# Kernel optimization log

Hardware: AMD Instinct MI355X
Metric: run time of the kernel (lower is better)

The kernel has to match this reference:

```python
import jax, jax.numpy as jnp
import numpy as np

D_IN = 1024
D_OUT = 1024
NUM_HEADS = 16
HEAD_DIM = D_OUT // NUM_HEADS
EPS = 1e-6
POW = 16.0


def setup_inputs() -> dict:
    key = jax.random.key(0)
    ks = jax.random.split(key, 6)
    s = 1.0 / np.sqrt(D_IN)
    x = jax.random.normal(ks[0], (2, 2048, D_IN), dtype=jnp.float32)
    Wq = jax.random.uniform(ks[1], (D_OUT, D_IN), jnp.float32, -s, s)
    Wk = jax.random.uniform(ks[2], (D_OUT, D_IN), jnp.float32, -s, s)
    Wv = jax.random.uniform(ks[3], (D_OUT, D_IN), jnp.float32, -s, s)
    Wo = jax.random.uniform(ks[4], (D_OUT, D_OUT), jnp.float32, -s, s)
    bo = jax.random.uniform(ks[5], (D_OUT,), jnp.float32, -s, s)
    return {"x": x, "Wq": Wq, "Wk": Wk, "Wv": Wv, "Wo": Wo, "bo": bo}


def _l2norm(t):
    # torch F.normalize: t / max(||t||, eps)
    n = jnp.sqrt(jnp.sum(t * t, axis=-1, keepdims=True))
    return t / jnp.maximum(n, EPS)


def reference(x, Wq, Wk, Wv, Wo, bo):
    B, T, _ = x.shape
    # project and split heads: [B, H, T, Dh]
    def heads(W):
        y = jnp.einsum('btd,od->bto', x, W)
        return y.reshape(B, T, NUM_HEADS, HEAD_DIM).transpose(0, 2, 1, 3)
    Q = _l2norm(heads(Wq))
    K = _l2norm(heads(Wk))
    V = heads(Wv)
    cos_sim = jnp.clip(jnp.einsum('bhtd,bhsd->bhts', Q, K), -0.999, 0.999)
    scores = 1.0 - jnp.arccos(cos_sim) / jnp.pi
    W = jnp.power(jnp.maximum(scores, EPS), POW)
    W = W / (jnp.sum(W, axis=-1, keepdims=True) + EPS)
    out = jnp.einsum('bhts,bhsd->bhtd', W, V)
    out = out.transpose(0, 2, 1, 3).reshape(B, T, D_OUT)
    return jnp.einsum('bto,po->btp', out, Wo) + bo
```

## Files before the change

kernel.cpp:

```cpp
#include <hip/hip_runtime.h>
#include <math.h>

constexpr int Dm   = 1024;
constexpr int NH   = 16;
constexpr int HD   = 64;
constexpr int Bb   = 2;
constexpr int Tt   = 2048;
constexpr int MTOT = Bb * Tt;
#define EPSF 1e-6f

typedef __attribute__((ext_vector_type(8))) short short8;
typedef __attribute__((ext_vector_type(4))) float f32x4;
typedef __attribute__((ext_vector_type(2))) float f32x2;

__device__ __forceinline__ ushort f2bf(float f) {
    union { float f; unsigned u; } v; v.f = f;
    unsigned r = (v.u + 0x7FFFu + ((v.u >> 16) & 1u)) >> 16;
    return (ushort)r;
}

__device__ __forceinline__ unsigned cvt_pk_bf16(float lo, float hi) {
    unsigned r;
    asm("v_cvt_pk_bf16_f32 %0, %1, %2" : "=v"(r) : "v"(lo), "v"(hi));
    return r;
}

__device__ __forceinline__ void gload16(const void* g, void* l) {
    __builtin_amdgcn_global_load_lds(
        (const __attribute__((address_space(1))) unsigned int*)g,
        (__attribute__((address_space(3))) unsigned int*)l,
        16, 0, 0);
}

__global__ __launch_bounds__(256)
void cvt_all(const float* __restrict__ x,  const float* __restrict__ wq,
             const float* __restrict__ wk, const float* __restrict__ wv,
             const float* __restrict__ wo,
             ushort* __restrict__ xb,  ushort* __restrict__ wqb,
             ushort* __restrict__ wkb, ushort* __restrict__ wvb,
             ushort* __restrict__ wob) {
    int i = blockIdx.x * 256 + threadIdx.x;
    const float* src; ushort* dst; int off;
    if (i < 1048576)      { src = x;  dst = xb;  off = i; }
    else if (i < 1310720) { src = wq; dst = wqb; off = i - 1048576; }
    else if (i < 1572864) { src = wk; dst = wkb; off = i - 1310720; }
    else if (i < 1835008) { src = wv; dst = wvb; off = i - 1572864; }
    else                  { src = wo; dst = wob; off = i - 1835008; }
    const float4 v = ((const float4*)src)[off];
    ushort4 o;
    o.x = f2bf(v.x); o.y = f2bf(v.y); o.z = f2bf(v.z); o.w = f2bf(v.w);
    ((ushort4*)dst)[off] = o;
}

template<bool OUTF32>
__device__ __forceinline__
void gemm_core(const ushort* __restrict__ A, const ushort* __restrict__ W,
               const float* __restrict__ bias, void* __restrict__ out,
               int m0, int n0, int N, int K, int mode) {
    __shared__ ushort As[128 * 64];
    __shared__ ushort Bs[128 * 64];
    const int tid  = threadIdx.x;
    const int wave = tid >> 6, lane = tid & 63;
    const int quad = lane >> 4, l15 = lane & 15;
    const int wr = wave >> 1, wc = wave & 1;
    const int lr = lane >> 3;
    const int sc = (lane & 7) ^ lr;

    f32x4 acc[4][4] = {};
    const ushort* Ab = A + (size_t)(m0 + lr) * K + sc * 8;
    const ushort* Wb = W + (size_t)(n0 + lr) * K + sc * 8;

    for (int k0 = 0; k0 < K; k0 += 64) {
        #pragma unroll
        for (int i = 0; i < 4; i++) {
            const int rows8 = (wave * 4 + i) * 8;
            gload16(Ab + (size_t)rows8 * K + k0, &As[rows8 * 64]);
            gload16(Wb + (size_t)rows8 * K + k0, &Bs[rows8 * 64]);
        }
        __syncthreads();
        #pragma unroll
        for (int kh = 0; kh < 2; kh++) {
            short8 af[4];
            #pragma unroll
            for (int mi = 0; mi < 4; mi++) {
                const int row = wr * 64 + mi * 16 + l15;
                af[mi] = *(const short8*)&As[row * 64 + (((kh * 4 + quad) ^ (row & 7)) * 8)];
            }
            #pragma unroll
            for (int nj = 0; nj < 4; nj++) {
                const int row = wc * 64 + nj * 16 + l15;
                const short8 bf = *(const short8*)&Bs[row * 64 + (((kh * 4 + quad) ^ (row & 7)) * 8)];
                #pragma unroll
                for (int mi = 0; mi < 4; mi++)
                    acc[mi][nj] = __builtin_amdgcn_mfma_f32_16x16x32_bf16(af[mi], bf, acc[mi][nj], 0, 0, 0);
            }
        }
        __syncthreads();
    }

    if (!OUTF32 && mode == 2) {
        #pragma unroll
        for (int mi = 0; mi < 4; mi++) {
            const int t  = m0 + wr * 64 + mi * 16 + quad * 4;
            const int bb = t >> 11, tl = t & 2047;
            #pragma unroll
            for (int nj = 0; nj < 4; nj++) {
                const int n = n0 + wc * 64 + nj * 16 + l15;
                const int hh = n >> 6, dd = n & 63;
                uint2 pk;
                pk.x = (unsigned)f2bf(acc[mi][nj][0]) | ((unsigned)f2bf(acc[mi][nj][1]) << 16);
                pk.y = (unsigned)f2bf(acc[mi][nj][2]) | ((unsigned)f2bf(acc[mi][nj][3]) << 16);
                *(uint2*)&((ushort*)out)[(size_t)((bb * NH + hh) * HD + dd) * Tt + tl] = pk;
            }
        }
        return;
    }

    #pragma unroll
    for (int mi = 0; mi < 4; mi++) {
        float inv[4] = {1.f, 1.f, 1.f, 1.f};
        if (!OUTF32 && mode == 1) {
            #pragma unroll
            for (int r = 0; r < 4; r++) {
                float ss = 0.f;
                #pragma unroll
                for (int nj = 0; nj < 4; nj++) ss += acc[mi][nj][r] * acc[mi][nj][r];
                ss += __shfl_xor(ss, 1); ss += __shfl_xor(ss, 2);
                ss += __shfl_xor(ss, 4); ss += __shfl_xor(ss, 8);
                inv[r] = 1.f / fmaxf(sqrtf(ss), EPSF);
            }
        }
        #pragma unroll
        for (int nj = 0; nj < 4; nj++)
            #pragma unroll
            for (int r = 0; r < 4; r++) {
                const int row = m0 + wr * 64 + mi * 16 + quad * 4 + r;
                const int col = n0 + wc * 64 + nj * 16 + l15;
                if (OUTF32)
                    ((float*)out)[(size_t)row * N + col] = acc[mi][nj][r] + bias[col];
                else
                    ((ushort*)out)[(size_t)row * N + col] = f2bf(acc[mi][nj][r] * inv[r]);
            }
    }
}

__global__ __launch_bounds__(256)
void qkv_gemm(const ushort* __restrict__ xb,
              const ushort* __restrict__ wq, const ushort* __restrict__ wk,
              const ushort* __restrict__ wv,
              ushort* __restrict__ qb, ushort* __restrict__ kb,
              ushort* __restrict__ vtb) {
    const int ny = blockIdx.y, sel = ny >> 3;
    const ushort* W = (sel == 0) ? wq : (sel == 1) ? wk : wv;
    ushort* out     = (sel == 0) ? qb : (sel == 1) ? kb : vtb;
    gemm_core<false>(xb, W, nullptr, out, blockIdx.x * 128, (ny & 7) * 128,
                     Dm, Dm, (sel < 2) ? 1 : 2);
}

__global__ __launch_bounds__(256)
void out_gemm(const ushort* __restrict__ A, const ushort* __restrict__ W,
              const float* __restrict__ bias, float* __restrict__ out) {
    __shared__ ushort As[64 * 64];
    __shared__ ushort Bs[128 * 64];
    const int tid  = threadIdx.x;
    const int wave = tid >> 6, lane = tid & 63;
    const int quad = lane >> 4, l15 = lane & 15;
    const int wm = wave & 1, wn = wave >> 1;
    const int lr = lane >> 3;
    const int sc = (lane & 7) ^ lr;
    const int m0 = blockIdx.x * 64, n0 = blockIdx.y * 128;
    const int K = Dm, N = Dm;

    f32x4 acc[2][4] = {};
    const ushort* Ab = A + (size_t)(m0 + lr) * K + sc * 8;
    const ushort* Wb = W + (size_t)(n0 + lr) * K + sc * 8;

    for (int k0 = 0; k0 < K; k0 += 64) {
        #pragma unroll
        for (int i = 0; i < 2; i++) {
            const int rows8 = (wave * 2 + i) * 8;
            gload16(Ab + (size_t)rows8 * K + k0, &As[rows8 * 64]);
        }
        #pragma unroll
        for (int i = 0; i < 4; i++) {
            const int rows8 = (wave * 4 + i) * 8;
            gload16(Wb + (size_t)rows8 * K + k0, &Bs[rows8 * 64]);
        }
        __syncthreads();
        #pragma unroll
        for (int kh = 0; kh < 2; kh++) {
            short8 af[2];
            #pragma unroll
            for (int mi = 0; mi < 2; mi++) {
                const int row = wm * 32 + mi * 16 + l15;
                af[mi] = *(const short8*)&As[row * 64 + (((kh * 4 + quad) ^ (row & 7)) * 8)];
            }
            #pragma unroll
            for (int nj = 0; nj < 4; nj++) {
                const int row = wn * 64 + nj * 16 + l15;
                const short8 bf = *(const short8*)&Bs[row * 64 + (((kh * 4 + quad) ^ (row & 7)) * 8)];
                #pragma unroll
                for (int mi = 0; mi < 2; mi++)
                    acc[mi][nj] = __builtin_amdgcn_mfma_f32_16x16x32_bf16(af[mi], bf, acc[mi][nj], 0, 0, 0);
            }
        }
        __syncthreads();
    }
    #pragma unroll
    for (int mi = 0; mi < 2; mi++)
        #pragma unroll
        for (int nj = 0; nj < 4; nj++)
            #pragma unroll
            for (int r = 0; r < 4; r++) {
                const int row = m0 + wm * 32 + mi * 16 + quad * 4 + r;
                const int col = n0 + wn * 64 + nj * 16 + l15;
                out[(size_t)row * N + col] = acc[mi][nj][r] + bias[col];
            }
}

__global__ __launch_bounds__(256)
void attn_kernel(const ushort* __restrict__ Qb, const ushort* __restrict__ Kb,
                 const ushort* __restrict__ Vtb, ushort* __restrict__ Ob) {
    __shared__ ushort Ks[2][64 * 64];
    __shared__ ushort Vs[2][64 * 64];
    const int tid  = threadIdx.x;
    const int wave = tid >> 6, lane = tid & 63;
    const int quad = lane >> 4, l15 = lane & 15;
    const int t0 = blockIdx.x * 64, h = blockIdx.y, b = blockIdx.z;

    const size_t qrow = (size_t)(b * Tt + t0 + 16 * wave + l15) * Dm + h * HD;
    const short8 qf0 = *(const short8*)&Qb[qrow + quad * 8];
    const short8 qf1 = *(const short8*)&Qb[qrow + 32 + quad * 8];

    const size_t kbase  = (size_t)(b * Tt) * Dm + h * HD;
    const size_t vtbase = (size_t)((b * NH + h) * HD) * Tt;
    const int r0 = tid >> 3, ch0 = tid & 7;
    const ushort* kg = Kb  + kbase  + (size_t)r0 * Dm + ch0 * 8;
    const ushort* vg = Vtb + vtbase + (size_t)r0 * Tt + ch0 * 8;
    const int lsw0 = r0 * 64 + ((ch0 ^ (r0 & 7)) * 8);
    const int lsw1 = (r0 + 32) * 64 + ((ch0 ^ (r0 & 7)) * 8);

    f32x4 oacc[4] = {};
    f32x2 denp = {0.f, 0.f};

    const f32x2 h3 = { 0.011180f,  0.011180f};
    const f32x2 h2 = {-0.002070f, -0.002070f};
    const f32x2 h1 = { 0.040732f,  0.040732f};
    const f32x2 h0 = { 0.450158f,  0.450158f};

    short8 pk0 = *(const short8*)kg;
    short8 pk1 = *(const short8*)(kg + (size_t)32 * Dm);
    short8 pv0 = *(const short8*)vg;
    short8 pv1 = *(const short8*)(vg + (size_t)32 * Tt);
    *(short8*)&Ks[0][lsw0] = pk0;  *(short8*)&Ks[0][lsw1] = pk1;
    *(short8*)&Vs[0][lsw0] = pv0;  *(short8*)&Vs[0][lsw1] = pv1;
    __syncthreads();

    const ushort* kgp = kg + (size_t)64 * Dm;
    const ushort* vgp = vg + 64;

    for (int i = 0; i < 32; i++) {
        const int p = i & 1;
        if (i < 31) {
            pk0 = *(const short8*)kgp;
            pk1 = *(const short8*)(kgp + (size_t)32 * Dm);
            pv0 = *(const short8*)vgp;
            pv1 = *(const short8*)(vgp + (size_t)32 * Tt);
            kgp += (size_t)64 * Dm;
            vgp += 64;
        }

        f32x4 sfT[4] = {};
        #pragma unroll
        for (int j = 0; j < 4; j++) {
            const int row = 16 * j + l15;
            const short8 kf0 = *(const short8*)&Ks[p][row * 64 + ((quad ^ (row & 7)) * 8)];
            const short8 kf1 = *(const short8*)&Ks[p][row * 64 + (((4 + quad) ^ (row & 7)) * 8)];
            sfT[j] = __builtin_amdgcn_mfma_f32_16x16x32_bf16(kf0, qf0, sfT[j], 0, 0, 0);
            sfT[j] = __builtin_amdgcn_mfma_f32_16x16x32_bf16(kf1, qf1, sfT[j], 0, 0, 0);
        }

        f32x2 wA[4], wB[4];
        #pragma unroll
        for (int r = 0; r < 4; r++) {
            f32x2 tA, tB;
            tA.x = __builtin_amdgcn_fmed3f(1.0f - sfT[0][r], 0.001f, 1.999f);
            tA.y = __builtin_amdgcn_fmed3f(1.0f - sfT[1][r], 0.001f, 1.999f);
            tB.x = __builtin_amdgcn_fmed3f(1.0f - sfT[2][r], 0.001f, 1.999f);
            tB.y = __builtin_amdgcn_fmed3f(1.0f - sfT[3][r], 0.001f, 1.999f);
            f32x2 pa = __builtin_elementwise_fma(tA, h3, h2);
            f32x2 pb = __builtin_elementwise_fma(tB, h3, h2);
            pa = __builtin_elementwise_fma(pa, tA, h1);
            pb = __builtin_elementwise_fma(pb, tB, h1);
            pa = __builtin_elementwise_fma(pa, tA, h0);
            pb = __builtin_elementwise_fma(pb, tB, h0);
            f32x2 ra, rb;
            ra.x = __builtin_amdgcn_sqrtf(tA.x); ra.y = __builtin_amdgcn_sqrtf(tA.y);
            rb.x = __builtin_amdgcn_sqrtf(tB.x); rb.y = __builtin_amdgcn_sqrtf(tB.y);
            const f32x2 one2 = {1.0f, 1.0f};
            f32x2 wa = __builtin_elementwise_fma(-ra, pa, one2);
            f32x2 wb = __builtin_elementwise_fma(-rb, pb, one2);
            wa *= wa; wa *= wa; wa *= wa; wa *= wa;
            wb *= wb; wb *= wb; wb *= wb; wb *= wb;
            denp += wa; denp += wb;
            wA[r] = wa; wB[r] = wb;
        }

        unsigned L0 = cvt_pk_bf16(wA[0].x, wA[1].x);
        unsigned L1 = cvt_pk_bf16(wA[0].y, wA[1].y);
        unsigned H0 = cvt_pk_bf16(wA[2].x, wA[3].x);
        unsigned H1 = cvt_pk_bf16(wA[2].y, wA[3].y);
        asm("v_permlane32_swap_b32 %0, %1" : "+v"(L0), "+v"(L1));
        asm("v_permlane16_swap_b32 %0, %1" : "+v"(L0), "+v"(L1));
        asm("v_permlane32_swap_b32 %0, %1" : "+v"(H0), "+v"(H1));
        asm("v_permlane16_swap_b32 %0, %1" : "+v"(H0), "+v"(H1));
        int4 bi1; bi1.x = (int)L0; bi1.y = (int)H0; bi1.z = (int)L1; bi1.w = (int)H1;
        const short8 Bf1 = __builtin_bit_cast(short8, bi1);
        unsigned L2 = cvt_pk_bf16(wB[0].x, wB[1].x);
        unsigned L3 = cvt_pk_bf16(wB[0].y, wB[1].y);
        unsigned H2 = cvt_pk_bf16(wB[2].x, wB[3].x);
        unsigned H3 = cvt_pk_bf16(wB[2].y, wB[3].y);
        asm("v_permlane32_swap_b32 %0, %1" : "+v"(L2), "+v"(L3));
        asm("v_permlane16_swap_b32 %0, %1" : "+v"(L2), "+v"(L3));
        asm("v_permlane32_swap_b32 %0, %1" : "+v"(H2), "+v"(H3));
        asm("v_permlane16_swap_b32 %0, %1" : "+v"(H2), "+v"(H3));
        int4 bi2; bi2.x = (int)L2; bi2.y = (int)H2; bi2.z = (int)L3; bi2.w = (int)H3;
        const short8 Bf2 = __builtin_bit_cast(short8, bi2);

        #pragma unroll
        for (int jd = 0; jd < 4; jd++) {
            const int vrow = 16 * jd + l15;
            const short8 vf0 = *(const short8*)&Vs[p][vrow * 64 + ((quad ^ (vrow & 7)) * 8)];
            const short8 vf1 = *(const short8*)&Vs[p][vrow * 64 + (((4 + quad) ^ (vrow & 7)) * 8)];
            oacc[jd] = __builtin_amdgcn_mfma_f32_16x16x32_bf16(vf0, Bf1, oacc[jd], 0, 0, 0);
            oacc[jd] = __builtin_amdgcn_mfma_f32_16x16x32_bf16(vf1, Bf2, oacc[jd], 0, 0, 0);
        }

        if (i < 31) {
            *(short8*)&Ks[1 - p][lsw0] = pk0;  *(short8*)&Ks[1 - p][lsw1] = pk1;
            *(short8*)&Vs[1 - p][lsw0] = pv0;  *(short8*)&Vs[1 - p][lsw1] = pv1;
        }
        __syncthreads();
    }

    float d = denp.x + denp.y;
    d += __shfl_xor(d, 16);
    d += __shfl_xor(d, 32);
    const float inv = __builtin_amdgcn_rcpf(d + EPSF);

    const size_t orow = (size_t)(b * Tt + t0 + 16 * wave + l15) * Dm + h * HD;
    #pragma unroll
    for (int jd = 0; jd < 4; jd++) {
        uint2 pk;
        pk.x = cvt_pk_bf16(oacc[jd][0] * inv, oacc[jd][1] * inv);
        pk.y = cvt_pk_bf16(oacc[jd][2] * inv, oacc[jd][3] * inv);
        *(uint2*)&Ob[orow + 16 * jd + quad * 4] = pk;
    }
}

extern "C" void kernel_launch(void* const* d_in, const int* in_sizes, int n_in,
                              void* d_out, int out_size, void* d_ws, size_t ws_size,
                              hipStream_t stream) {
    const float* x  = (const float*)d_in[0];
    const float* Wq = (const float*)d_in[1];
    const float* Wk = (const float*)d_in[2];
    const float* Wv = (const float*)d_in[3];
    const float* Wo = (const float*)d_in[4];
    const float* bo = (const float*)d_in[5];
    float* out = (float*)d_out;

    ushort* ws = (ushort*)d_ws;
    const size_t M1 = 1u << 20;
    ushort* xb  = ws;
    ushort* wqb = ws + 4 * M1;
    ushort* wkb = ws + 5 * M1;
    ushort* wvb = ws + 6 * M1;
    ushort* wob = ws + 7 * M1;
    ushort* qb  = ws + 8 * M1;
    ushort* kb  = ws + 12 * M1;
    ushort* vtb = ws + 16 * M1;
    ushort* aob = ws + 20 * M1;

    cvt_all<<<8192, 256, 0, stream>>>(x, Wq, Wk, Wv, Wo, xb, wqb, wkb, wvb, wob);
    qkv_gemm<<<dim3(MTOT / 128, 24), 256, 0, stream>>>(xb, wqb, wkb, wvb, qb, kb, vtb);
    attn_kernel<<<dim3(Tt / 64, NH, Bb), 256, 0, stream>>>(qb, kb, vtb, aob);
    out_gemm<<<dim3(MTOT / 64, Dm / 128), 256, 0, stream>>>(aob, wob, bo, out);
}
```

Before: 219.7 us.

## Split attention key range across two wave teams and merge partial outputs

The attention kernel now runs 512 threads, organised as two teams of four waves. Each team processes half of the key/value sequence with 32-key tiles instead of 64-key tiles. At the end, team 1 writes its partial output and denominators to shared memory, and team 0 adds them in before normalising and storing. This doubles parallelism per query block and shortens each wave's serial loop, to hide latency and raise occupancy. The cost is an extra shared-memory reduction, smaller MFMA batches per iteration, and block-wide syncs that now span eight waves.

```diff
diff --git a/kernel.cpp b/kernel.cpp
--- a/kernel.cpp
+++ b/kernel.cpp
@@ -218,27 +218,31 @@
             }
 }
 
-__global__ __launch_bounds__(256)
+__global__ __launch_bounds__(512, 8)
 void attn_kernel(const ushort* __restrict__ Qb, const ushort* __restrict__ Kb,
                  const ushort* __restrict__ Vtb, ushort* __restrict__ Ob) {
-    __shared__ ushort Ks[2][64 * 64];
-    __shared__ ushort Vs[2][64 * 64];
+    __shared__ char smem[32768 + 256];
     const int tid  = threadIdx.x;
     const int wave = tid >> 6, lane = tid & 63;
+    const int team = wave >> 2, wq = wave & 3;
     const int quad = lane >> 4, l15 = lane & 15;
     const int t0 = blockIdx.x * 64, h = blockIdx.y, b = blockIdx.z;
-
-    const size_t qrow = (size_t)(b * Tt + t0 + 16 * wave + l15) * Dm + h * HD;
+    const int tb = team << 14;
+
+    const size_t qrow = (size_t)(b * Tt + t0 + 16 * wq + l15) * Dm + h * HD;
     const short8 qf0 = *(const short8*)&Qb[qrow + quad * 8];
     const short8 qf1 = *(const short8*)&Qb[qrow + 32 + quad * 8];
 
+    const int tt   = tid & 255;
+    const int r0k  = tt >> 3, ch0k = tt & 7;
+    const int r0v  = tt >> 2, ch0v = tt & 3;
+    const int lswK = r0k * 64 + ((ch0k ^ (r0k & 7)) * 8);
+    const int lswV = r0v * 32 + ((ch0v ^ (r0v & 3)) * 8);
+
     const size_t kbase  = (size_t)(b * Tt) * Dm + h * HD;
     const size_t vtbase = (size_t)((b * NH + h) * HD) * Tt;
-    const int r0 = tid >> 3, ch0 = tid & 7;
-    const ushort* kg = Kb  + kbase  + (size_t)r0 * Dm + ch0 * 8;
-    const ushort* vg = Vtb + vtbase + (size_t)r0 * Tt + ch0 * 8;
-    const int lsw0 = r0 * 64 + ((ch0 ^ (r0 & 7)) * 8);
-    const int lsw1 = (r0 + 32) * 64 + ((ch0 ^ (r0 & 7)) * 8);
+    const ushort* kg = Kb  + kbase  + (size_t)(team * 1024 + r0k) * Dm + ch0k * 8;
+    const ushort* vg = Vtb + vtbase + (size_t)r0v * Tt + team * 1024 + ch0v * 8;
 
     f32x4 oacc[4] = {};
     f32x2 denp = {0.f, 0.f};
@@ -249,61 +253,51 @@
     const f32x2 h0 = { 0.450158f,  0.450158f};
 
     short8 pk0 = *(const short8*)kg;
-    short8 pk1 = *(const short8*)(kg + (size_t)32 * Dm);
     short8 pv0 = *(const short8*)vg;
-    short8 pv1 = *(const short8*)(vg + (size_t)32 * Tt);
-    *(short8*)&Ks[0][lsw0] = pk0;  *(short8*)&Ks[0][lsw1] = pk1;
-    *(short8*)&Vs[0][lsw0] = pv0;  *(short8*)&Vs[0][lsw1] = pv1;
+    *(short8*)((char*)smem + tb + lswK * 2) = pk0;
+    *(short8*)((char*)smem + tb + 8192 + lswV * 2) = pv0;
     __syncthreads();
 
-    const ushort* kgp = kg + (size_t)64 * Dm;
-    const ushort* vgp = vg + 64;
+    const ushort* kgp = kg + (size_t)32 * Dm;
+    const ushort* vgp = vg + 32;
 
     for (int i = 0; i < 32; i++) {
         const int p = i & 1;
+        const ushort* Kp = (const ushort*)(smem + tb + (p << 12));
+        const ushort* Vp = (const ushort*)(smem + tb + 8192 + (p << 12));
         if (i < 31) {
             pk0 = *(const short8*)kgp;
-            pk1 = *(const short8*)(kgp + (size_t)32 * Dm);
             pv0 = *(const short8*)vgp;
-            pv1 = *(const short8*)(vgp + (size_t)32 * Tt);
-            kgp += (size_t)64 * Dm;
-            vgp += 64;
-        }
-
-        f32x4 sfT[4] = {};
-        #pragma unroll
-        for (int j = 0; j < 4; j++) {
+            kgp += (size_t)32 * Dm;
+            vgp += 32;
+        }
+
+        f32x4 sfT[2] = {};
+        #pragma unroll
+        for (int j = 0; j < 2; j++) {
             const int row = 16 * j + l15;
-            const short8 kf0 = *(const short8*)&Ks[p][row * 64 + ((quad ^ (row & 7)) * 8)];
-            const short8 kf1 = *(const short8*)&Ks[p][row * 64 + (((4 + quad) ^ (row & 7)) * 8)];
+            const short8 kf0 = *(const short8*)&Kp[row * 64 + ((quad ^ (row & 7)) * 8)];
+            const short8 kf1 = *(const short8*)&Kp[row * 64 + (((4 + quad) ^ (row & 7)) * 8)];
             sfT[j] = __builtin_amdgcn_mfma_f32_16x16x32_bf16(kf0, qf0, sfT[j], 0, 0, 0);
             sfT[j] = __builtin_amdgcn_mfma_f32_16x16x32_bf16(kf1, qf1, sfT[j], 0, 0, 0);
         }
 
-        f32x2 wA[4], wB[4];
+        f32x2 wA[4];
         #pragma unroll
         for (int r = 0; r < 4; r++) {
-            f32x2 tA, tB;
+            f32x2 tA;
             tA.x = __builtin_amdgcn_fmed3f(1.0f - sfT[0][r], 0.001f, 1.999f);
             tA.y = __builtin_amdgcn_fmed3f(1.0f - sfT[1][r], 0.001f, 1.999f);
-            tB.x = __builtin_amdgcn_fmed3f(1.0f - sfT[2][r], 0.001f, 1.999f);
-            tB.y = __builtin_amdgcn_fmed3f(1.0f - sfT[3][r], 0.001f, 1.999f);
             f32x2 pa = __builtin_elementwise_fma(tA, h3, h2);
-            f32x2 pb = __builtin_elementwise_fma(tB, h3, h2);
             pa = __builtin_elementwise_fma(pa, tA, h1);
-            pb = __builtin_elementwise_fma(pb, tB, h1);
             pa = __builtin_elementwise_fma(pa, tA, h0);
-            pb = __builtin_elementwise_fma(pb, tB, h0);
-            f32x2 ra, rb;
+            f32x2 ra;
             ra.x = __builtin_amdgcn_sqrtf(tA.x); ra.y = __builtin_amdgcn_sqrtf(tA.y);
-            rb.x = __builtin_amdgcn_sqrtf(tB.x); rb.y = __builtin_amdgcn_sqrtf(tB.y);
             const f32x2 one2 = {1.0f, 1.0f};
             f32x2 wa = __builtin_elementwise_fma(-ra, pa, one2);
-            f32x2 wb = __builtin_elementwise_fma(-rb, pb, one2);
             wa *= wa; wa *= wa; wa *= wa; wa *= wa;
-            wb *= wb; wb *= wb; wb *= wb; wb *= wb;
-            denp += wa; denp += wb;
-            wA[r] = wa; wB[r] = wb;
+            denp += wa;
+            wA[r] = wa;
         }
 
         unsigned L0 = cvt_pk_bf16(wA[0].x, wA[1].x);
@@ -316,29 +310,17 @@
         asm("v_permlane16_swap_b32 %0, %1" : "+v"(H0), "+v"(H1));
         int4 bi1; bi1.x = (int)L0; bi1.y = (int)H0; bi1.z = (int)L1; bi1.w = (int)H1;
         const short8 Bf1 = __builtin_bit_cast(short8, bi1);
-        unsigned L2 = cvt_pk_bf16(wB[0].x, wB[1].x);
-        unsigned L3 = cvt_pk_bf16(wB[0].y, wB[1].y);
-        unsigned H2 = cvt_pk_bf16(wB[2].x, wB[3].x);
-        unsigned H3 = cvt_pk_bf16(wB[2].y, wB[3].y);
-        asm("v_permlane32_swap_b32 %0, %1" : "+v"(L2), "+v"(L3));
-        asm("v_permlane16_swap_b32 %0, %1" : "+v"(L2), "+v"(L3));
-        asm("v_permlane32_swap_b32 %0, %1" : "+v"(H2), "+v"(H3));
-        asm("v_permlane16_swap_b32 %0, %1" : "+v"(H2), "+v"(H3));
-        int4 bi2; bi2.x = (int)L2; bi2.y = (int)H2; bi2.z = (int)L3; bi2.w = (int)H3;
-        const short8 Bf2 = __builtin_bit_cast(short8, bi2);
 
         #pragma unroll
         for (int jd = 0; jd < 4; jd++) {
             const int vrow = 16 * jd + l15;
-            const short8 vf0 = *(const short8*)&Vs[p][vrow * 64 + ((quad ^ (vrow & 7)) * 8)];
-            const short8 vf1 = *(const short8*)&Vs[p][vrow * 64 + (((4 + quad) ^ (vrow & 7)) * 8)];
-            oacc[jd] = __builtin_amdgcn_mfma_f32_16x16x32_bf16(vf0, Bf1, oacc[jd], 0, 0, 0);
-            oacc[jd] = __builtin_amdgcn_mfma_f32_16x16x32_bf16(vf1, Bf2, oacc[jd], 0, 0, 0);
+            const short8 vf = *(const short8*)&Vp[vrow * 32 + ((quad ^ (vrow & 3)) * 8)];
+            oacc[jd] = __builtin_amdgcn_mfma_f32_16x16x32_bf16(vf, Bf1, oacc[jd], 0, 0, 0);
         }
 
         if (i < 31) {
-            *(short8*)&Ks[1 - p][lsw0] = pk0;  *(short8*)&Ks[1 - p][lsw1] = pk1;
-            *(short8*)&Vs[1 - p][lsw0] = pv0;  *(short8*)&Vs[1 - p][lsw1] = pv1;
+            *(short8*)((char*)smem + tb + ((1 - p) << 12) + lswK * 2) = pk0;
+            *(short8*)((char*)smem + tb + 8192 + ((1 - p) << 12) + lswV * 2) = pv0;
         }
         __syncthreads();
     }
@@ -346,15 +328,35 @@
     float d = denp.x + denp.y;
     d += __shfl_xor(d, 16);
     d += __shfl_xor(d, 32);
-    const float inv = __builtin_amdgcn_rcpf(d + EPSF);
-
-    const size_t orow = (size_t)(b * Tt + t0 + 16 * wave + l15) * Dm + h * HD;
-    #pragma unroll
-    for (int jd = 0; jd < 4; jd++) {
-        uint2 pk;
-        pk.x = cvt_pk_bf16(oacc[jd][0] * inv, oacc[jd][1] * inv);
-        pk.y = cvt_pk_bf16(oacc[jd][2] * inv, oacc[jd][3] * inv);
-        *(uint2*)&Ob[orow + 16 * jd + quad * 4] = pk;
+
+    float* Obuf = (float*)smem;
+    float* Den  = (float*)(smem + 32768);
+    const int q = 16 * wq + l15;
+
+    if (team == 1) {
+        #pragma unroll
+        for (int jd = 0; jd < 4; jd++)
+            #pragma unroll
+            for (int r = 0; r < 4; r++)
+                Obuf[q * 64 + 16 * jd + quad * 4 + r] = oacc[jd][r];
+        if (quad == 0) Den[q] = d;
+    }
+    __syncthreads();
+
+    if (team == 0) {
+        const float inv = __builtin_amdgcn_rcpf(d + Den[q] + EPSF);
+        const size_t orow = (size_t)(b * Tt + t0 + q) * Dm + h * HD;
+        #pragma unroll
+        for (int jd = 0; jd < 4; jd++) {
+            float o0 = (oacc[jd][0] + Obuf[q * 64 + 16 * jd + quad * 4 + 0]) * inv;
+            float o1 = (oacc[jd][1] + Obuf[q * 64 + 16 * jd + quad * 4 + 1]) * inv;
+            float o2 = (oacc[jd][2] + Obuf[q * 64 + 16 * jd + quad * 4 + 2]) * inv;
+            float o3 = (oacc[jd][3] + Obuf[q * 64 + 16 * jd + quad * 4 + 3]) * inv;
+            uint2 pk2;
+            pk2.x = cvt_pk_bf16(o0, o1);
+            pk2.y = cvt_pk_bf16(o2, o3);
+            *(uint2*)&Ob[orow + 16 * jd + quad * 4] = pk2;
+        }
     }
 }
 
@@ -383,6 +385,6 @@
 
     cvt_all<<<8192, 256, 0, stream>>>(x, Wq, Wk, Wv, Wo, xb, wqb, wkb, wvb, wob);
     qkv_gemm<<<dim3(MTOT / 128, 24), 256, 0, stream>>>(xb, wqb, wkb, wvb, qb, kb, vtb);
-    attn_kernel<<<dim3(Tt / 64, NH, Bb), 256, 0, stream>>>(qb, kb, vtb, aob);
+    attn_kernel<<<dim3(Tt / 64, NH, Bb), 512, 0, stream>>>(qb, kb, vtb, aob);
     out_gemm<<<dim3(MTOT / 64, Dm / 128), 256, 0, stream>>>(aob, wob, bo, out);
 }
```

Measured after the change: 224.2 us. +2.0%, slower.
